# Kernel optimization log

Measured on AMD Instinct MI355X. Metric: run time of the kernel, lower is better.

## Reference

```python
import jax, jax.numpy as jnp
import numpy as np

B, S, D, H = 2, 4096, 512, 8
DH = D // H

def setup_inputs() -> dict:
    key = jax.random.key(0)
    k_enc, kq, kk, kv, ko = jax.random.split(key, 5)
    xavier = float(np.sqrt(6.0 / (D + D)))
    enc = jax.random.normal(k_enc, (B, S, D), dtype=jnp.float32)
    W_Q = jax.random.uniform(kq, (D, D), jnp.float32, -xavier, xavier)
    W_K = jax.random.uniform(kk, (D, D), jnp.float32, -xavier, xavier)
    W_V = jax.random.uniform(kv, (D, D), jnp.float32, -xavier, xavier)
    W_O = jax.random.uniform(ko, (D, D), jnp.float32, -xavier, xavier)
    # lower-triangular causal mask, broadcast over batch and heads
    causal_mask = jnp.tril(jnp.ones((S, S), dtype=jnp.int32))[None, None]
    return {"enc": enc, "causal_mask": causal_mask,
            "W_Q": W_Q, "W_K": W_K, "W_V": W_V, "W_O": W_O}

def reference(enc, causal_mask, W_Q, W_K, W_V, W_O):
    b, s, _ = enc.shape
    q = (enc @ W_Q).reshape(b, s, H, DH).transpose(0, 2, 1, 3)  # [b,h,s,dh]
    k = (enc @ W_K).reshape(b, s, H, DH).transpose(0, 2, 1, 3)
    v = (enc @ W_V).reshape(b, s, H, DH).transpose(0, 2, 1, 3)
    scores = jnp.einsum('bhqd,bhkd->bhqk', q, k) / jnp.sqrt(jnp.float32(DH))
    scores = jnp.where(causal_mask == 0, -jnp.inf, scores)
    attn = jax.nn.softmax(scores, axis=-1)
    out = jnp.einsum('bhqk,bhkd->bhqd', attn, v)  # [b,h,s,dh]
    concat = out.transpose(0, 2, 1, 3).reshape(b, s, H * DH)
    return concat @ W_O
```

## Files before the change

kernel.cpp:

```cpp
#include <hip/hip_runtime.h>


typedef _Float16 f16x8 __attribute__((ext_vector_type(8)));
typedef float f32x16 __attribute__((ext_vector_type(16)));

__device__ __forceinline__ f32x16 mma32(f16x8 a, f16x8 b, f32x16 c) {
  return __builtin_amdgcn_mfma_f32_32x32x16_f16(a, b, c, 0, 0, 0);
}

__device__ __forceinline__ void gload16(const void* g, void* l) {
  __builtin_amdgcn_global_load_lds((const __attribute__((address_space(1))) void*)g,
                                   (__attribute__((address_space(3))) void*)l, 16, 0, 0);
}

__global__ __launch_bounds__(256) void prep_k(const float* __restrict__ enc,
                                              const float* __restrict__ WQ,
                                              const float* __restrict__ WK,
                                              const float* __restrict__ WV,
                                              const float* __restrict__ WO,
                                              _Float16* __restrict__ enc16,
                                              _Float16* __restrict__ WtQ,
                                              _Float16* __restrict__ WtK,
                                              _Float16* __restrict__ WtV,
                                              _Float16* __restrict__ WtO) {
  const int bid = blockIdx.x;
  if (bid < 2048) {
    const size_t i = (size_t)bid * 256 + threadIdx.x;
    const float4* p = (const float4*)(enc + i * 8);
    const float4 a = p[0], b = p[1];
    union { f16x8 v; uint4 u; } r;
    r.v[0] = (_Float16)a.x; r.v[1] = (_Float16)a.y; r.v[2] = (_Float16)a.z; r.v[3] = (_Float16)a.w;
    r.v[4] = (_Float16)b.x; r.v[5] = (_Float16)b.y; r.v[6] = (_Float16)b.z; r.v[7] = (_Float16)b.w;
    *(uint4*)(enc16 + i * 8) = r.u;
  } else {
    const int t = bid - 2048;
    const int wsel = t >> 8;
    const float* W = (wsel == 0) ? WQ : (wsel == 1) ? WK : (wsel == 2) ? WV : WO;
    _Float16* T = (wsel == 0) ? WtQ : (wsel == 1) ? WtK : (wsel == 2) ? WtV : WtO;
    const int tb = t & 255;
    const int k0 = (tb & 15) * 32, n0 = (tb >> 4) * 32;
    __shared__ float tt[32][33];
    const int c = threadIdx.x & 31, r8 = threadIdx.x >> 5;
#pragma unroll
    for (int p = 0; p < 4; ++p) tt[c][r8 + 8 * p] = W[(size_t)(k0 + r8 + 8 * p) * 512 + n0 + c];
    __syncthreads();
#pragma unroll
    for (int p = 0; p < 4; ++p)
      T[(size_t)(n0 + r8 + 8 * p) * 512 + k0 + c] = (_Float16)tt[r8 + 8 * p][c];
  }
}

__device__ __forceinline__ void gemm_core(const _Float16* __restrict__ A,
                                          const _Float16* __restrict__ Wt,
                                          int m0, int n0,
                                          _Float16* Al, _Float16* Bl,
                                          f32x16 acc[2][2]) {
  const int tid = threadIdx.x, w = tid >> 6, l = tid & 63;
  const int hi = l >> 5, li = l & 31;
  const int wm = w >> 1, wn = w & 1;
  const int srow = l >> 3, sunit = (l & 7) ^ (l >> 3);
  const int arow = 32 * w;

#pragma unroll
  for (int mb = 0; mb < 2; ++mb)
#pragma unroll
    for (int nb = 0; nb < 2; ++nb)
#pragma unroll
      for (int r = 0; r < 16; ++r) acc[mb][nb][r] = 0.f;

#pragma unroll
  for (int i = 0; i < 4; ++i) {
    gload16(A + (size_t)(m0 + arow + 8 * i + srow) * 512 + sunit * 8, Al + (arow + 8 * i) * 64);
    gload16(Wt + (size_t)(n0 + arow + 8 * i + srow) * 512 + sunit * 8, Bl + (arow + 8 * i) * 64);
  }
  for (int kk = 0; kk < 8; ++kk) {
    const int cur = kk & 1;
    __syncthreads();
    if (kk < 7) {
      const int kn = (kk + 1) * 64;
#pragma unroll
      for (int i = 0; i < 4; ++i) {
        gload16(A + (size_t)(m0 + arow + 8 * i + srow) * 512 + kn + sunit * 8,
                Al + (cur ^ 1) * 8192 + (arow + 8 * i) * 64);
        gload16(Wt + (size_t)(n0 + arow + 8 * i + srow) * 512 + kn + sunit * 8,
                Bl + (cur ^ 1) * 8192 + (arow + 8 * i) * 64);
      }
    }
#pragma unroll
    for (int ks = 0; ks < 4; ++ks) {
      f16x8 af[2], bf[2];
#pragma unroll
      for (int mb = 0; mb < 2; ++mb)
        af[mb] = *(const f16x8*)((const char*)(Al + cur * 8192 + (64 * wm + 32 * mb + li) * 64) +
                                 (((2 * ks + hi) ^ (li & 7)) << 4));
#pragma unroll
      for (int nb = 0; nb < 2; ++nb)
        bf[nb] = *(const f16x8*)((const char*)(Bl + cur * 8192 + (64 * wn + 32 * nb + li) * 64) +
                                 (((2 * ks + hi) ^ (li & 7)) << 4));
#pragma unroll
      for (int mb = 0; mb < 2; ++mb)
#pragma unroll
        for (int nb = 0; nb < 2; ++nb) acc[mb][nb] = mma32(af[mb], bf[nb], acc[mb][nb]);
    }
  }
}

__global__ __launch_bounds__(256) void qkv_k(const _Float16* __restrict__ A,
                                             const _Float16* __restrict__ WtQ,
                                             const _Float16* __restrict__ WtK,
                                             const _Float16* __restrict__ WtV,
                                             _Float16* __restrict__ Qw,
                                             _Float16* __restrict__ Kw,
                                             _Float16* __restrict__ Vpw,
                                             float qscale) {
  __shared__ __align__(16) _Float16 Al[2 * 128 * 64];
  __shared__ __align__(16) _Float16 Bl[2 * 128 * 64];
  const int m0 = blockIdx.x * 128;
  const int wid = blockIdx.y >> 2, n0 = (blockIdx.y & 3) * 128;
  const _Float16* Wt = (wid == 0) ? WtQ : (wid == 1) ? WtK : WtV;
  f32x16 acc[2][2];
  gemm_core(A, Wt, m0, n0, Al, Bl, acc);

  const int tid = threadIdx.x, w = tid >> 6, l = tid & 63;
  const int hi = l >> 5, li = l & 31;
  const int wm = w >> 1, wn = w & 1;
  if (wid < 2) {
    _Float16* Cp = (wid == 0) ? Qw : Kw;
    const float scale = (wid == 0) ? qscale : 1.f;
#pragma unroll
    for (int mb = 0; mb < 2; ++mb)
#pragma unroll
      for (int nb = 0; nb < 2; ++nb)
#pragma unroll
        for (int r = 0; r < 16; ++r) {
          const int m = m0 + 64 * wm + 32 * mb + (r & 3) + 8 * (r >> 2) + 4 * hi;
          const int n = n0 + 64 * wn + 32 * nb + li;
          const int b = m >> 12, s = m & 4095, h = n >> 6, d = n & 63;
          Cp[((((size_t)b * 8 + h) * 4096 + s) << 6) + d] = (_Float16)(acc[mb][nb][r] * scale);
        }
  } else {
#pragma unroll
    for (int mb = 0; mb < 2; ++mb)
#pragma unroll
      for (int nb = 0; nb < 2; ++nb)
#pragma unroll
        for (int c = 0; c < 4; ++c) {
          const int mbase = m0 + 64 * wm + 32 * mb + 16 * (c >> 1);
          const int n = n0 + 64 * wn + 32 * nb + li;
          const int b = mbase >> 12, sb = mbase & 4095, h = n >> 6, d = n & 63;
          union { uint2 u; _Float16 h4[4]; } t4;
#pragma unroll
          for (int t = 0; t < 4; ++t) t4.h4[t] = (_Float16)acc[mb][nb][4 * c + t];
          *(uint2*)(Vpw + ((((size_t)b * 8 + h) * 64 + d) << 12) + sb + 4 * (c & 1) + 8 * hi) = t4.u;
        }
  }
}

__global__ __launch_bounds__(256) void fgemm_k(const _Float16* __restrict__ A,
                                               const _Float16* __restrict__ Wt,
                                               float* __restrict__ out) {
  __shared__ __align__(16) _Float16 Al[2 * 128 * 64];
  __shared__ __align__(16) _Float16 Bl[2 * 128 * 64];
  const int m0 = blockIdx.x * 128, n0 = blockIdx.y * 128;
  f32x16 acc[2][2];
  gemm_core(A, Wt, m0, n0, Al, Bl, acc);
  const int tid = threadIdx.x, w = tid >> 6, l = tid & 63;
  const int hi = l >> 5, li = l & 31;
  const int wm = w >> 1, wn = w & 1;
#pragma unroll
  for (int mb = 0; mb < 2; ++mb)
#pragma unroll
    for (int nb = 0; nb < 2; ++nb)
#pragma unroll
      for (int r = 0; r < 16; ++r) {
        const int m = m0 + 64 * wm + 32 * mb + (r & 3) + 8 * (r >> 2) + 4 * hi;
        const int n = n0 + 64 * wn + 32 * nb + li;
        out[(size_t)m * 512 + n] = acc[mb][nb][r];
      }
}

__global__ __launch_bounds__(256) void flash_k(const _Float16* __restrict__ Q,
                                               const _Float16* __restrict__ K,
                                               const _Float16* __restrict__ Vp,
                                               _Float16* __restrict__ att,
                                               _Float16* __restrict__ pO,
                                               float2* __restrict__ ml) {
  __shared__ __align__(16) _Float16 Kl[2 * 64 * 64];
  __shared__ __align__(16) _Float16 Vl[2 * 64 * 64];

  const int u = blockIdx.x;
  const int bh = u & 15;
  const int j = 67 - (u >> 4);
  int qt, cc;
  if (j < 10) { qt = j; cc = 0; }
  else if (j < 30) { qt = 10 + ((j - 10) >> 1); cc = (j - 10) & 1; }
  else if (j < 60) { qt = 20 + (j - 30) / 3; cc = (j - 30) % 3; }
  else { qt = 30 + ((j - 60) >> 2); cc = (j - 60) & 3; }
  const int nt = 2 * qt + 2;
  const int ktlo = 20 * cc;
  const int kthi = min(ktlo + 19, nt - 1);
  const bool split = (nt > 20);
  const int q0 = qt * 128;
  const int tid = threadIdx.x, w = tid >> 6, l = tid & 63;
  const int hi = l >> 5, li = l & 31;
  const int srow = l >> 3, sunit = (l & 7) ^ (l >> 3);

  const size_t bhoff = (size_t)bh * 4096 * 64;
  const _Float16* Kb = K + bhoff;
  const _Float16* Vb = Vp + bhoff;
  const _Float16* Qb = Q + bhoff;
  const int qg = q0 + 32 * w + li;

  f16x8 qB[4];
#pragma unroll
  for (int ks = 0; ks < 4; ++ks)
    qB[ks] = *(const f16x8*)(Qb + (size_t)qg * 64 + 16 * ks + 8 * hi);

  f32x16 o2[2], lacc;
#pragma unroll
  for (int db = 0; db < 2; ++db)
#pragma unroll
    for (int r = 0; r < 16; ++r) o2[db][r] = 0.f;
#pragma unroll
  for (int r = 0; r < 16; ++r) lacc[r] = 0.f;
  float m_ = -__builtin_inff();

#pragma unroll
  for (int e = 0; e < 2; ++e) {
    const int row = 16 * w + 8 * e;
    gload16(Kb + (size_t)(ktlo * 64 + row + srow) * 64 + sunit * 8, Kl + row * 64);
    gload16(Vb + (size_t)(row + srow) * 4096 + ktlo * 64 + sunit * 8, Vl + row * 64);
  }

  for (int kt = ktlo; kt <= kthi; ++kt) {
    const int cur = kt & 1;
    __syncthreads();
    if (kt < kthi) {
      const int k0n = (kt + 1) * 64;
#pragma unroll
      for (int e = 0; e < 2; ++e) {
        const int row = 16 * w + 8 * e;
        gload16(Kb + (size_t)(k0n + row + srow) * 64 + sunit * 8,
                Kl + (cur ^ 1) * 4096 + row * 64);
        gload16(Vb + (size_t)(row + srow) * 4096 + k0n + sunit * 8,
                Vl + (cur ^ 1) * 4096 + row * 64);
      }
    }

    f32x16 s2[2];
#pragma unroll
    for (int kb = 0; kb < 2; ++kb)
#pragma unroll
      for (int r = 0; r < 16; ++r) s2[kb][r] = 0.f;
    __builtin_amdgcn_s_setprio(1);
#pragma unroll
    for (int ks = 0; ks < 4; ++ks)
#pragma unroll
      for (int kb = 0; kb < 2; ++kb) {
        const f16x8 kf = *(const f16x8*)((const char*)(Kl + cur * 4096 + (32 * kb + li) * 64) +
                                         (((2 * ks + hi) ^ (li & 7)) << 4));
        s2[kb] = mma32(kf, qB[ks], s2[kb]);
      }
    __builtin_amdgcn_s_setprio(0);

    if (kt >= 2 * qt) {
      const int limit = qg - kt * 64;
#pragma unroll
      for (int kb = 0; kb < 2; ++kb)
#pragma unroll
        for (int r = 0; r < 16; ++r) {
          const int kl = 32 * kb + (r & 3) + 8 * (r >> 2) + 4 * hi;
          if (kl > limit) s2[kb][r] = -__builtin_inff();
        }
    }

#define RV(i) s2[(i) >> 4][(i) & 15]
    float a[11];
#pragma unroll
    for (int i = 0; i < 10; ++i)
      a[i] = fmaxf(fmaxf(RV(3 * i), RV(3 * i + 1)), RV(3 * i + 2));
    a[10] = fmaxf(RV(30), RV(31));
#undef RV
    float b4[4];
    b4[0] = fmaxf(fmaxf(a[0], a[1]), a[2]);
    b4[1] = fmaxf(fmaxf(a[3], a[4]), a[5]);
    b4[2] = fmaxf(fmaxf(a[6], a[7]), a[8]);
    b4[3] = fmaxf(a[9], a[10]);
    const float mxl = fmaxf(fmaxf(fmaxf(b4[0], b4[1]), b4[2]), b4[3]);

    if (!__all(mxl <= m_ + 8.f)) {
      const float vm = fmaxf(mxl, __shfl_xor(mxl, 32, 64));
      const float mn = fmaxf(m_, vm);
      const float al = __builtin_amdgcn_exp2f(m_ - mn);
      m_ = mn;
#pragma unroll
      for (int r = 0; r < 16; ++r) lacc[r] *= al;
#pragma unroll
      for (int db = 0; db < 2; ++db)
#pragma unroll
        for (int r = 0; r < 16; ++r) o2[db][r] *= al;
    }
#pragma unroll
    for (int kb = 0; kb < 2; ++kb)
#pragma unroll
      for (int r = 0; r < 16; ++r) s2[kb][r] = __builtin_amdgcn_exp2f(s2[kb][r] - m_);
#pragma unroll
    for (int kb = 0; kb < 2; ++kb)
#pragma unroll
      for (int r = 0; r < 16; ++r) lacc[r] += s2[kb][r];

    f16x8 pb[4];
#pragma unroll
    for (int ks = 0; ks < 4; ++ks) {
      union { f16x8 v; unsigned int u[4]; } pu;
      const int kb = ks >> 1, base = 8 * (ks & 1);
#pragma unroll
      for (int p2 = 0; p2 < 4; ++p2)
        pu.u[p2] = __builtin_bit_cast(unsigned int,
                     __builtin_amdgcn_cvt_pkrtz(s2[kb][base + 2 * p2], s2[kb][base + 2 * p2 + 1]));
      pb[ks] = pu.v;
    }

    __builtin_amdgcn_s_setprio(1);
#pragma unroll
    for (int ks = 0; ks < 4; ++ks)
#pragma unroll
      for (int db = 0; db < 2; ++db) {
        const f16x8 vf = *(const f16x8*)((const char*)(Vl + cur * 4096 + (32 * db + li) * 64) +
                                         (((2 * ks + hi) ^ (li & 7)) << 4));
        o2[db] = mma32(vf, pb[ks], o2[db]);
      }
    __builtin_amdgcn_s_setprio(0);
  }

  float t8[8];
#pragma unroll
  for (int i = 0; i < 8; ++i) t8[i] = lacc[i] + lacc[i + 8];
  float lsum = ((t8[0] + t8[1]) + (t8[2] + t8[3])) + ((t8[4] + t8[5]) + (t8[6] + t8[7]));
  lsum += __shfl_xor(lsum, 32, 64);
  const float inv = 1.f / lsum;
  if (!split) {
    const int b = bh >> 3, h = bh & 7;
    _Float16* op = att + ((size_t)b * 4096 + qg) * 512 + h * 64;
#pragma unroll
    for (int db = 0; db < 2; ++db)
#pragma unroll
      for (int c = 0; c < 4; ++c) {
        union { uint2 u; _Float16 h4[4]; } t4;
#pragma unroll
        for (int t = 0; t < 4; ++t) t4.h4[t] = (_Float16)(o2[db][4 * c + t] * inv);
        *(uint2*)(op + 32 * db + 8 * c + 4 * hi) = t4.u;
      }
  } else {
    int off;
    if (qt < 20) off = (qt - 10) * 2;
    else if (qt < 30) off = 20 + (qt - 20) * 3;
    else off = 50 + (qt - 30) * 4;
    const int slot = bh * 58 + off + cc;
    const int qrow = 32 * w + li;
    _Float16* op = pO + (size_t)slot * 8192 + qrow * 64;
#pragma unroll
    for (int db = 0; db < 2; ++db)
#pragma unroll
      for (int c = 0; c < 4; ++c) {
        union { uint2 u; _Float16 h4[4]; } t4;
#pragma unroll
        for (int t = 0; t < 4; ++t) t4.h4[t] = (_Float16)(o2[db][4 * c + t] * inv);
        *(uint2*)(op + 32 * db + 8 * c + 4 * hi) = t4.u;
      }
    if (hi == 0) ml[slot * 128 + qrow] = make_float2(m_, lsum);
  }
}

__global__ __launch_bounds__(256) void combine_k(const float2* __restrict__ ml,
                                                 const _Float16* __restrict__ pO,
                                                 _Float16* __restrict__ att) {
  const int tid = threadIdx.x;
  const int rid = blockIdx.x * 8 + (tid >> 5);
  const int d2 = tid & 31;
  const int bh = rid / 2816, rem = rid % 2816;
  const int qt = 10 + (rem >> 7), qrow = rem & 127;
  const int nc = (qt < 20) ? 2 : (qt < 30) ? 3 : 4;
  int off;
  if (qt < 20) off = (qt - 10) * 2;
  else if (qt < 30) off = 20 + (qt - 20) * 3;
  else off = 50 + (qt - 30) * 4;
  const int slot0 = bh * 58 + off;

  float2 mlc[4];
  float M = -__builtin_inff();
#pragma unroll
  for (int c = 0; c < 4; ++c)
    if (c < nc) {
      mlc[c] = ml[(slot0 + c) * 128 + qrow];
      M = fmaxf(M, mlc[c].x);
    }
  float wc[4], wsum = 0.f;
#pragma unroll
  for (int c = 0; c < 4; ++c)
    if (c < nc) {
      wc[c] = __builtin_amdgcn_exp2f(mlc[c].x - M) * mlc[c].y;
      wsum += wc[c];
    }
  const float inv = 1.f / wsum;
  float acc0 = 0.f, acc1 = 0.f;
#pragma unroll
  for (int c = 0; c < 4; ++c)
    if (c < nc) {
      union { unsigned int u; _Float16 h2[2]; } x;
      x.u = *(const unsigned int*)(pO + (size_t)(slot0 + c) * 8192 + qrow * 64 + 2 * d2);
      const float a = wc[c] * inv;
      acc0 += (float)x.h2[0] * a;
      acc1 += (float)x.h2[1] * a;
    }
  union { unsigned int u; _Float16 h2[2]; } y;
  y.h2[0] = (_Float16)acc0;
  y.h2[1] = (_Float16)acc1;
  const int b = bh >> 3, h = bh & 7, q = qt * 128 + qrow;
  *(unsigned int*)(att + ((size_t)b * 4096 + q) * 512 + h * 64 + 2 * d2) = y.u;
}

extern "C" void kernel_launch(void* const* d_in, const int* in_sizes, int n_in,
                              void* d_out, int out_size, void* d_ws, size_t ws_size,
                              hipStream_t stream) {
  const float* enc = (const float*)d_in[0];
  const float* WQ = (const float*)d_in[2];
  const float* WK = (const float*)d_in[3];
  const float* WV = (const float*)d_in[4];
  const float* WO = (const float*)d_in[5];
  float* out = (float*)d_out;

  const size_t NE = (size_t)2 * 8 * 4096 * 64;
  _Float16* enc16 = (_Float16*)d_ws;
  _Float16* Qw = enc16 + NE;
  _Float16* Kw = Qw + NE;
  _Float16* Vpw = Kw + NE;
  _Float16* WtQ = Vpw + NE;
  _Float16* WtK = WtQ + 512 * 512;
  _Float16* WtV = WtK + 512 * 512;
  _Float16* WtO = WtV + 512 * 512;
  _Float16* att = WtO + 512 * 512;
  float2* ml = (float2*)enc16;
  _Float16* pO = (_Float16*)d_out;

  prep_k<<<3072, 256, 0, stream>>>(enc, WQ, WK, WV, WO, enc16, WtQ, WtK, WtV, WtO);
  qkv_k<<<dim3(64, 12), 256, 0, stream>>>(enc16, WtQ, WtK, WtV, Qw, Kw, Vpw, 0.1803368801f);
  flash_k<<<1088, 256, 0, stream>>>(Qw, Kw, Vpw, att, pO, ml);
  combine_k<<<5632, 256, 0, stream>>>(ml, pO, att);
  fgemm_k<<<dim3(64, 4), 256, 0, stream>>>(att, WtO, out);
}
```

Baseline: 122.7 us.

## Load K/V fragments directly from global memory into registers in flash kernel

Drops the shared-memory double-buffered K/V staging (global_load_lds plus a __syncthreads per tile) from the flash attention kernel. Each wave now loads its MFMA K and V fragments straight from global memory into registers at the start of every tile. This removes LDS traffic and block-wide barriers and frees LDS. In exchange, the four waves each read the same K/V tile redundantly from global/L2, and the loads are no longer prefetched a tile ahead, so load latency is exposed unless the compiler hoists them.

```diff
diff --git a/kernel.cpp b/kernel.cpp
--- a/kernel.cpp
+++ b/kernel.cpp
@@ -185,9 +185,6 @@
                                                _Float16* __restrict__ att,
                                                _Float16* __restrict__ pO,
                                                float2* __restrict__ ml) {
-  __shared__ __align__(16) _Float16 Kl[2 * 64 * 64];
-  __shared__ __align__(16) _Float16 Vl[2 * 64 * 64];
-
   const int u = blockIdx.x;
   const int bh = u & 15;
   const int j = 67 - (u >> 4);
@@ -203,7 +200,6 @@
   const int q0 = qt * 128;
   const int tid = threadIdx.x, w = tid >> 6, l = tid & 63;
   const int hi = l >> 5, li = l & 31;
-  const int srow = l >> 3, sunit = (l & 7) ^ (l >> 3);
 
   const size_t bhoff = (size_t)bh * 4096 * 64;
   const _Float16* Kb = K + bhoff;
@@ -216,6 +212,9 @@
   for (int ks = 0; ks < 4; ++ks)
     qB[ks] = *(const f16x8*)(Qb + (size_t)qg * 64 + 16 * ks + 8 * hi);
 
+  const _Float16* Kfb = Kb + (size_t)li * 64 + 8 * hi;
+  const _Float16* Vfb = Vb + (size_t)li * 4096 + 8 * hi;
+
   f32x16 o2[2], lacc;
 #pragma unroll
   for (int db = 0; db < 2; ++db)
@@ -225,27 +224,20 @@
   for (int r = 0; r < 16; ++r) lacc[r] = 0.f;
   float m_ = -__builtin_inff();
 
-#pragma unroll
-  for (int e = 0; e < 2; ++e) {
-    const int row = 16 * w + 8 * e;
-    gload16(Kb + (size_t)(ktlo * 64 + row + srow) * 64 + sunit * 8, Kl + row * 64);
-    gload16(Vb + (size_t)(row + srow) * 4096 + ktlo * 64 + sunit * 8, Vl + row * 64);
-  }
-
   for (int kt = ktlo; kt <= kthi; ++kt) {
-    const int cur = kt & 1;
-    __syncthreads();
-    if (kt < kthi) {
-      const int k0n = (kt + 1) * 64;
-#pragma unroll
-      for (int e = 0; e < 2; ++e) {
-        const int row = 16 * w + 8 * e;
-        gload16(Kb + (size_t)(k0n + row + srow) * 64 + sunit * 8,
-                Kl + (cur ^ 1) * 4096 + row * 64);
-        gload16(Vb + (size_t)(row + srow) * 4096 + k0n + sunit * 8,
-                Vl + (cur ^ 1) * 4096 + row * 64);
-      }
-    }
+    const int k0 = kt * 64;
+
+    f16x8 kf[8], vf[8];
+#pragma unroll
+    for (int ks = 0; ks < 4; ++ks)
+#pragma unroll
+      for (int kb = 0; kb < 2; ++kb)
+        kf[2 * ks + kb] = *(const f16x8*)(Kfb + (size_t)(k0 + 32 * kb) * 64 + 16 * ks);
+#pragma unroll
+    for (int ks = 0; ks < 4; ++ks)
+#pragma unroll
+      for (int db = 0; db < 2; ++db)
+        vf[2 * ks + db] = *(const f16x8*)(Vfb + (size_t)(32 * db) * 4096 + k0 + 16 * ks);
 
     f32x16 s2[2];
 #pragma unroll
@@ -256,11 +248,8 @@
 #pragma unroll
     for (int ks = 0; ks < 4; ++ks)
 #pragma unroll
-      for (int kb = 0; kb < 2; ++kb) {
-        const f16x8 kf = *(const f16x8*)((const char*)(Kl + cur * 4096 + (32 * kb + li) * 64) +
-                                         (((2 * ks + hi) ^ (li & 7)) << 4));
-        s2[kb] = mma32(kf, qB[ks], s2[kb]);
-      }
+      for (int kb = 0; kb < 2; ++kb)
+        s2[kb] = mma32(kf[2 * ks + kb], qB[ks], s2[kb]);
     __builtin_amdgcn_s_setprio(0);
 
     if (kt >= 2 * qt) {
@@ -325,11 +314,8 @@
 #pragma unroll
     for (int ks = 0; ks < 4; ++ks)
 #pragma unroll
-      for (int db = 0; db < 2; ++db) {
-        const f16x8 vf = *(const f16x8*)((const char*)(Vl + cur * 4096 + (32 * db + li) * 64) +
-                                         (((2 * ks + hi) ^ (li & 7)) << 4));
-        o2[db] = mma32(vf, pb[ks], o2[db]);
-      }
+      for (int db = 0; db < 2; ++db)
+        o2[db] = mma32(vf[2 * ks + db], pb[ks], o2[db]);
     __builtin_amdgcn_s_setprio(0);
   }
 
```

Measured after the change: 206.3 us. +68.2%, slower.

## Load K/V in 128-key pairs per barrier instead of double-buffered 64-key tiles

Applied to the files above, without the earlier changes.

Replaces the double-buffered 64-key K/V pipeline with a single 128-key LDS buffer that is loaded in one shot, followed by a barrier and two 64-key tile steps. V uses a wider 128-column swizzled layout. This halves the number of barriers per key range but drops the prefetch overlap, so global loads are no longer hidden behind MFMA work. It also assumes the tile count in each chunk is even.

```diff
diff --git a/kernel.cpp b/kernel.cpp
--- a/kernel.cpp
+++ b/kernel.cpp
@@ -185,8 +185,8 @@
                                                _Float16* __restrict__ att,
                                                _Float16* __restrict__ pO,
                                                float2* __restrict__ ml) {
-  __shared__ __align__(16) _Float16 Kl[2 * 64 * 64];
-  __shared__ __align__(16) _Float16 Vl[2 * 64 * 64];
+  __shared__ __align__(16) _Float16 Kl[128 * 64];
+  __shared__ __align__(16) _Float16 Vl[64 * 128];
 
   const int u = blockIdx.x;
   const int bh = u & 15;
@@ -203,7 +203,6 @@
   const int q0 = qt * 128;
   const int tid = threadIdx.x, w = tid >> 6, l = tid & 63;
   const int hi = l >> 5, li = l & 31;
-  const int srow = l >> 3, sunit = (l & 7) ^ (l >> 3);
 
   const size_t bhoff = (size_t)bh * 4096 * 64;
   const _Float16* Kb = K + bhoff;
@@ -225,28 +224,7 @@
   for (int r = 0; r < 16; ++r) lacc[r] = 0.f;
   float m_ = -__builtin_inff();
 
-#pragma unroll
-  for (int e = 0; e < 2; ++e) {
-    const int row = 16 * w + 8 * e;
-    gload16(Kb + (size_t)(ktlo * 64 + row + srow) * 64 + sunit * 8, Kl + row * 64);
-    gload16(Vb + (size_t)(row + srow) * 4096 + ktlo * 64 + sunit * 8, Vl + row * 64);
-  }
-
-  for (int kt = ktlo; kt <= kthi; ++kt) {
-    const int cur = kt & 1;
-    __syncthreads();
-    if (kt < kthi) {
-      const int k0n = (kt + 1) * 64;
-#pragma unroll
-      for (int e = 0; e < 2; ++e) {
-        const int row = 16 * w + 8 * e;
-        gload16(Kb + (size_t)(k0n + row + srow) * 64 + sunit * 8,
-                Kl + (cur ^ 1) * 4096 + row * 64);
-        gload16(Vb + (size_t)(row + srow) * 4096 + k0n + sunit * 8,
-                Vl + (cur ^ 1) * 4096 + row * 64);
-      }
-    }
-
+  auto tile_step = [&](int kt, int half) {
     f32x16 s2[2];
 #pragma unroll
     for (int kb = 0; kb < 2; ++kb)
@@ -257,8 +235,9 @@
     for (int ks = 0; ks < 4; ++ks)
 #pragma unroll
       for (int kb = 0; kb < 2; ++kb) {
-        const f16x8 kf = *(const f16x8*)((const char*)(Kl + cur * 4096 + (32 * kb + li) * 64) +
-                                         (((2 * ks + hi) ^ (li & 7)) << 4));
+        const f16x8 kf = *(const f16x8*)(
+            (const char*)(Kl + (64 * half + 32 * kb + li) * 64) +
+            (((2 * ks + hi) ^ (li & 7)) << 4));
         s2[kb] = mma32(kf, qB[ks], s2[kb]);
       }
     __builtin_amdgcn_s_setprio(0);
@@ -326,11 +305,36 @@
     for (int ks = 0; ks < 4; ++ks)
 #pragma unroll
       for (int db = 0; db < 2; ++db) {
-        const f16x8 vf = *(const f16x8*)((const char*)(Vl + cur * 4096 + (32 * db + li) * 64) +
-                                         (((2 * ks + hi) ^ (li & 7)) << 4));
+        const f16x8 vf = *(const f16x8*)(
+            (const char*)(Vl + (32 * db + li) * 128) +
+            ((((8 * half + 2 * ks + hi)) ^ (li & 15)) << 4));
         o2[db] = mma32(vf, pb[ks], o2[db]);
       }
     __builtin_amdgcn_s_setprio(0);
+  };
+
+  const int npair = (kthi - ktlo + 1) >> 1;
+  for (int p = 0; p < npair; ++p) {
+    const int kt0 = ktlo + 2 * p;
+    const int k0 = kt0 * 64;
+    if (p) __syncthreads();
+#pragma unroll
+    for (int e = 0; e < 4; ++e) {
+      const int kr = 32 * w + 8 * e;
+      gload16(Kb + (size_t)(k0 + kr + (l >> 3)) * 64 + (((l & 7) ^ ((l >> 3) & 7)) << 3),
+              Kl + kr * 64);
+    }
+#pragma unroll
+    for (int e = 0; e < 4; ++e) {
+      const int vr = 16 * w + 4 * e;
+      gload16(Vb + (size_t)(vr + (l >> 4)) * 4096 + k0 +
+                  ((((l & 15) ^ ((4 * e + (l >> 4)) & 15))) << 3),
+              Vl + vr * 128);
+    }
+    __syncthreads();
+
+    tile_step(kt0, 0);
+    tile_step(kt0 + 1, 1);
   }
 
   float t8[8];
```

Result: slower. 146.8 us (+19.6%).
